# Kernel optimization log

Measured on AMD Instinct MI355X. Metric: run time of the kernel, lower is better.

## Reference

```python
import jax, jax.numpy as jnp
import numpy as np


def setup_inputs() -> dict:
    key = jax.random.key(0)
    k1, k2, k3, k4 = jax.random.split(key, 4)
    S, B = 64000, 64
    audio = jax.random.normal(k1, (S, B), dtype=jnp.float32)
    g = jax.random.uniform(k2, (S, B, 1), dtype=jnp.float32)
    twoR = jax.random.uniform(k3, (S, B, 1), dtype=jnp.float32)
    mix = jax.random.uniform(k4, (S, B, 3), dtype=jnp.float32)
    return {"audio": audio, "g": g, "twoR": twoR, "mix": mix}


def reference(audio, g, twoR, mix):
    # audio: [S, B]; g, twoR: [S, B, 1]; mix: [S, B, 3]
    S, B = audio.shape
    T = 1.0 / (1.0 + g * (g + twoR))                      # [S, B, 1]
    ones = jnp.ones_like(g)
    # Time-varying 2x2 transition matrix H[t, b] = T * [[1, -g], [g, 2Rg+1]]
    H = T[..., None] * jnp.concatenate(
        [ones, -g, g, twoR * g + 1.0], axis=-1).reshape(S, B, 2, 2)
    gHB = g * T * jnp.concatenate([ones, g], axis=-1)     # [S, B, 2]
    gHBx = gHB * audio[..., None]                         # [S, B, 2]

    def step(state, inp):
        # state: [B, 2]; Ht: [B, 2, 2]; bt: [B, 2]
        Ht, bt = inp
        Yt = bt + jnp.einsum('bij,bj->bi', Ht, state)
        return 2.0 * Yt - state, Yt

    state0 = jnp.ones((B, 2), dtype=audio.dtype)
    _, Y = jax.lax.scan(step, state0, (H, gHBx))          # Y: [S, B, 2]

    twoR2 = twoR[..., 0]                                  # [S, B]
    y_hps = audio - twoR2 * Y[..., 0] - Y[..., 1]
    y_mixed = (twoR2 * mix[..., 0] * Y[..., 0]
               + mix[..., 1] * Y[..., 1]
               + mix[..., 2] * y_hps)
    return y_mixed.T                                      # [B, S]
```

## Files before the change

### kernel.cpp

```cpp
#include <hip/hip_runtime.h>

#define S_LEN  64000
#define B_N    64
#define MCH    8
#define WPB    8
#define BSTEPS (MCH * WPB)
#define NBLK   (S_LEN / BSTEPS)
#define KPL    4
#define SCAN_T 256

struct Aff { float m00, m01, m10, m11, v0, v1; };

__device__ __forceinline__ Aff aff_id() {
    Aff r; r.m00 = 1.f; r.m01 = 0.f; r.m10 = 0.f; r.m11 = 1.f; r.v0 = 0.f; r.v1 = 0.f;
    return r;
}

__device__ __forceinline__ Aff aff_comp(const Aff& X, const Aff& Y) {
    Aff r;
    r.m00 = fmaf(X.m00, Y.m00, X.m01 * Y.m10);
    r.m01 = fmaf(X.m00, Y.m01, X.m01 * Y.m11);
    r.m10 = fmaf(X.m10, Y.m00, X.m11 * Y.m10);
    r.m11 = fmaf(X.m10, Y.m01, X.m11 * Y.m11);
    r.v0  = fmaf(X.m00, Y.v0, fmaf(X.m01, Y.v1, X.v0));
    r.v1  = fmaf(X.m10, Y.v0, fmaf(X.m11, Y.v1, X.v1));
    return r;
}

__device__ __forceinline__ Aff svf_step(float g, float R, float x) {
    Aff a;
    float T  = 1.0f / fmaf(g, g + R, 1.0f);
    float gT = g * T;
    a.m00 = fmaf(2.0f, T, -1.0f);
    a.m01 = -2.0f * gT;
    a.m10 =  2.0f * gT;
    a.m11 = fmaf(2.0f, fmaf(R, gT, T), -1.0f);
    a.v0  = a.m10 * x;
    a.v1  = g * a.v0;
    return a;
}

__device__ __forceinline__ void aff_store_lds(float* p, const Aff& a) {
    p[0] = a.m00; p[1] = a.m01; p[2] = a.m10; p[3] = a.m11; p[4] = a.v0; p[5] = a.v1;
}
__device__ __forceinline__ Aff aff_load_lds(const float* p) {
    Aff a; a.m00 = p[0]; a.m01 = p[1]; a.m10 = p[2]; a.m11 = p[3]; a.v0 = p[4]; a.v1 = p[5];
    return a;
}
__device__ __forceinline__ void aff_store_g(float2* p, const Aff& a) {
    p[0] = make_float2(a.m00, a.m01);
    p[1] = make_float2(a.m10, a.m11);
    p[2] = make_float2(a.v0,  a.v1);
}
__device__ __forceinline__ Aff aff_load_g(const float2* p) {
    float2 x = p[0], y = p[1], z = p[2];
    Aff a; a.m00 = x.x; a.m01 = x.y; a.m10 = y.x; a.m11 = y.y; a.v0 = z.x; a.v1 = z.y;
    return a;
}

__global__ __launch_bounds__(512) void k_macro(
    const float* __restrict__ audio, const float* __restrict__ g,
    const float* __restrict__ twoR, float2* __restrict__ wsMac)
{
    __shared__ float affs[WPB * B_N * 7];
    const int b   = threadIdx.x & 63;
    const int w   = threadIdx.x >> 6;
    const int blk = blockIdx.x;
    const int base = (blk * BSTEPS + w * MCH) * B_N + b;

    Aff acc = aff_id();
#pragma unroll
    for (int i = 0; i < MCH; ++i) {
        const int idx = base + i * B_N;
        acc = aff_comp(svf_step(g[idx], twoR[idx], audio[idx]), acc);
    }
    aff_store_lds(&affs[(w * B_N + b) * 7], acc);
    __syncthreads();

    if (w == 0) {
        Aff M = acc;
#pragma unroll
        for (int j = 1; j < WPB; ++j) {
            Aff A = aff_load_lds(&affs[(j * B_N + b) * 7]);
            M = aff_comp(A, M);
        }
        aff_store_g(&wsMac[(blk * B_N + b) * 3], M);
    }
}

__global__ __launch_bounds__(SCAN_T) void k_scan(
    const float2* __restrict__ wsMac, float2* __restrict__ sIn)
{
    const int b    = blockIdx.x;
    const int t    = threadIdx.x;
    const int lane = t & 63;
    const int wave = t >> 6;

    Aff cM[KPL];
#pragma unroll
    for (int k = 0; k < KPL; ++k) {
        const int p = t * KPL + k;
        cM[k] = (p < NBLK) ? aff_load_g(&wsMac[(p * B_N + b) * 3]) : aff_id();
    }

    Aff acc = aff_id();
#pragma unroll
    for (int k = 0; k < KPL; ++k) acc = aff_comp(cM[k], acc);

#pragma unroll
    for (int d = 1; d < 64; d <<= 1) {
        Aff o;
        o.m00 = __shfl_up(acc.m00, (unsigned)d, 64);
        o.m01 = __shfl_up(acc.m01, (unsigned)d, 64);
        o.m10 = __shfl_up(acc.m10, (unsigned)d, 64);
        o.m11 = __shfl_up(acc.m11, (unsigned)d, 64);
        o.v0  = __shfl_up(acc.v0,  (unsigned)d, 64);
        o.v1  = __shfl_up(acc.v1,  (unsigned)d, 64);
        if (lane >= d) acc = aff_comp(acc, o);
    }

    __shared__ Aff wt[SCAN_T / 64];
    if (lane == 63) wt[wave] = acc;
    __syncthreads();

    Aff E;
    E.m00 = __shfl_up(acc.m00, 1u, 64);
    E.m01 = __shfl_up(acc.m01, 1u, 64);
    E.m10 = __shfl_up(acc.m10, 1u, 64);
    E.m11 = __shfl_up(acc.m11, 1u, 64);
    E.v0  = __shfl_up(acc.v0,  1u, 64);
    E.v1  = __shfl_up(acc.v1,  1u, 64);
    if (lane == 0) E = aff_id();

    Aff P = aff_id();
    for (int j = 0; j < wave; ++j) P = aff_comp(wt[j], P);
    E = aff_comp(E, P);

    float s0 = E.m00 + E.m01 + E.v0;
    float s1 = E.m10 + E.m11 + E.v1;

#pragma unroll
    for (int k = 0; k < KPL; ++k) {
        const int p = t * KPL + k;
        if (p < NBLK) {
            sIn[p * B_N + b] = make_float2(s0, s1);
            float n0 = fmaf(cM[k].m00, s0, fmaf(cM[k].m01, s1, cM[k].v0));
            float n1 = fmaf(cM[k].m10, s0, fmaf(cM[k].m11, s1, cM[k].v1));
            s0 = n0; s1 = n1;
        }
    }
}

__global__ __launch_bounds__(512) void k_replay(
    const float* __restrict__ audio, const float* __restrict__ g,
    const float* __restrict__ twoR, const float* __restrict__ mix,
    const float2* __restrict__ sIn, float* __restrict__ out)
{
    __shared__ float lds[BSTEPS * 65];
    const int b   = threadIdx.x & 63;
    const int w   = threadIdx.x >> 6;
    const int blk = blockIdx.x;
    const int base = (blk * BSTEPS + w * MCH) * B_N + b;

    float gv[MCH], Rv[MCH], xv[MCH], m0v[MCH], m1v[MCH], m2v[MCH];
#pragma unroll
    for (int i = 0; i < MCH; ++i) {
        const int idx = base + i * B_N;
        gv[i] = g[idx]; Rv[i] = twoR[idx]; xv[i] = audio[idx];
        m0v[i] = mix[idx * 3]; m1v[i] = mix[idx * 3 + 1]; m2v[i] = mix[idx * 3 + 2];
    }

    Aff acc = aff_id();
#pragma unroll
    for (int i = 0; i < MCH; ++i)
        acc = aff_comp(svf_step(gv[i], Rv[i], xv[i]), acc);
    aff_store_lds(&lds[(w * B_N + b) * 7], acc);
    __syncthreads();

    float2 sm = sIn[blk * B_N + b];
    Aff P = aff_id();
    for (int j = 0; j < w; ++j) {
        Aff A = aff_load_lds(&lds[(j * B_N + b) * 7]);
        P = aff_comp(A, P);
    }
    float s0 = fmaf(P.m00, sm.x, fmaf(P.m01, sm.y, P.v0));
    float s1 = fmaf(P.m10, sm.x, fmaf(P.m11, sm.y, P.v1));
    __syncthreads();

#pragma unroll
    for (int i = 0; i < MCH; ++i) {
        float gg = gv[i], R = Rv[i], x = xv[i];
        float T  = 1.0f / fmaf(gg, gg + R, 1.0f);
        float gT = gg * T;
        float b0 = gT * x;
        float b1 = gg * b0;
        float Y0 = fmaf(T, s0, fmaf(-gT, s1, b0));
        float Y1 = fmaf(gT, s0, fmaf(fmaf(R, gT, T), s1, b1));
        s0 = fmaf(2.0f, Y0, -s0);
        s1 = fmaf(2.0f, Y1, -s1);

        float yh = x - fmaf(R, Y0, Y1);
        float y  = fmaf(R * m0v[i], Y0, fmaf(m1v[i], Y1, m2v[i] * yh));

        lds[(w * MCH + i) * 65 + b] = y;
    }
    __syncthreads();

    const int col = threadIdx.x & 63;
    const int r0  = threadIdx.x >> 6;
    const int colbase = blk * BSTEPS;
#pragma unroll
    for (int r = r0; r < B_N; r += WPB) {
        out[r * S_LEN + colbase + col] = lds[col * 65 + r];
    }
}

extern "C" void kernel_launch(void* const* d_in, const int* in_sizes, int n_in,
                              void* d_out, int out_size, void* d_ws, size_t ws_size,
                              hipStream_t stream)
{
    const float* audio = (const float*)d_in[0];
    const float* g     = (const float*)d_in[1];
    const float* twoR  = (const float*)d_in[2];
    const float* mix   = (const float*)d_in[3];
    float* out = (float*)d_out;

    float2* wsMac = (float2*)d_ws;
    float2* sIn   = wsMac + NBLK * B_N * 3;

    k_macro <<<dim3(NBLK), dim3(512), 0, stream>>>(audio, g, twoR, wsMac);
    k_scan  <<<dim3(B_N), dim3(SCAN_T), 0, stream>>>(wsMac, sIn);
    k_replay<<<dim3(NBLK), dim3(512), 0, stream>>>(audio, g, twoR, mix, sIn, out);
}
```

Measured before the change: 37.73 us.

## Fuse macro, scan and replay passes into one cooperative kernel with grid syncs

```diff
diff --git a/kernel.cpp b/kernel.cpp
--- a/kernel.cpp
+++ b/kernel.cpp
@@ -1,13 +1,15 @@
 #include <hip/hip_runtime.h>
+#include <hip/hip_cooperative_groups.h>
+
+namespace cg = cooperative_groups;
 
 #define S_LEN  64000
 #define B_N    64
-#define MCH    8
-#define WPB    8
-#define BSTEPS (MCH * WPB)
+#define TPB    1024
+#define WPB    16
+#define MCH    16
+#define BSTEPS (WPB * MCH)
 #define NBLK   (S_LEN / BSTEPS)
-#define KPL    4
-#define SCAN_T 256
 
 struct Aff { float m00, m01, m10, m11, v0, v1; };
 
@@ -58,160 +60,126 @@
     return a;
 }
 
-__global__ __launch_bounds__(512) void k_macro(
+__global__ __launch_bounds__(TPB) void k_fused(
     const float* __restrict__ audio, const float* __restrict__ g,
-    const float* __restrict__ twoR, float2* __restrict__ wsMac)
+    const float* __restrict__ twoR, const float* __restrict__ mix,
+    float2* __restrict__ wsMac, float2* __restrict__ sEntry,
+    float* __restrict__ out)
 {
     __shared__ float affs[WPB * B_N * 7];
+    __shared__ float tile[128 * 65];
+    __shared__ Aff wt[4];
+
     const int b   = threadIdx.x & 63;
     const int w   = threadIdx.x >> 6;
     const int blk = blockIdx.x;
     const int base = (blk * BSTEPS + w * MCH) * B_N + b;
 
-    Aff acc = aff_id();
-#pragma unroll
-    for (int i = 0; i < MCH; ++i) {
-        const int idx = base + i * B_N;
-        acc = aff_comp(svf_step(g[idx], twoR[idx], audio[idx]), acc);
-    }
-    aff_store_lds(&affs[(w * B_N + b) * 7], acc);
-    __syncthreads();
-
-    if (w == 0) {
-        Aff M = acc;
-#pragma unroll
-        for (int j = 1; j < WPB; ++j) {
-            Aff A = aff_load_lds(&affs[(j * B_N + b) * 7]);
-            M = aff_comp(A, M);
-        }
-        aff_store_g(&wsMac[(blk * B_N + b) * 3], M);
-    }
-}
-
-__global__ __launch_bounds__(SCAN_T) void k_scan(
-    const float2* __restrict__ wsMac, float2* __restrict__ sIn)
-{
-    const int b    = blockIdx.x;
-    const int t    = threadIdx.x;
-    const int lane = t & 63;
-    const int wave = t >> 6;
-
-    Aff cM[KPL];
-#pragma unroll
-    for (int k = 0; k < KPL; ++k) {
-        const int p = t * KPL + k;
-        cM[k] = (p < NBLK) ? aff_load_g(&wsMac[(p * B_N + b) * 3]) : aff_id();
-    }
-
-    Aff acc = aff_id();
-#pragma unroll
-    for (int k = 0; k < KPL; ++k) acc = aff_comp(cM[k], acc);
-
-#pragma unroll
-    for (int d = 1; d < 64; d <<= 1) {
-        Aff o;
-        o.m00 = __shfl_up(acc.m00, (unsigned)d, 64);
-        o.m01 = __shfl_up(acc.m01, (unsigned)d, 64);
-        o.m10 = __shfl_up(acc.m10, (unsigned)d, 64);
-        o.m11 = __shfl_up(acc.m11, (unsigned)d, 64);
-        o.v0  = __shfl_up(acc.v0,  (unsigned)d, 64);
-        o.v1  = __shfl_up(acc.v1,  (unsigned)d, 64);
-        if (lane >= d) acc = aff_comp(acc, o);
-    }
-
-    __shared__ Aff wt[SCAN_T / 64];
-    if (lane == 63) wt[wave] = acc;
-    __syncthreads();
-
-    Aff E;
-    E.m00 = __shfl_up(acc.m00, 1u, 64);
-    E.m01 = __shfl_up(acc.m01, 1u, 64);
-    E.m10 = __shfl_up(acc.m10, 1u, 64);
-    E.m11 = __shfl_up(acc.m11, 1u, 64);
-    E.v0  = __shfl_up(acc.v0,  1u, 64);
-    E.v1  = __shfl_up(acc.v1,  1u, 64);
-    if (lane == 0) E = aff_id();
-
-    Aff P = aff_id();
-    for (int j = 0; j < wave; ++j) P = aff_comp(wt[j], P);
-    E = aff_comp(E, P);
-
-    float s0 = E.m00 + E.m01 + E.v0;
-    float s1 = E.m10 + E.m11 + E.v1;
-
-#pragma unroll
-    for (int k = 0; k < KPL; ++k) {
-        const int p = t * KPL + k;
-        if (p < NBLK) {
-            sIn[p * B_N + b] = make_float2(s0, s1);
-            float n0 = fmaf(cM[k].m00, s0, fmaf(cM[k].m01, s1, cM[k].v0));
-            float n1 = fmaf(cM[k].m10, s0, fmaf(cM[k].m11, s1, cM[k].v1));
-            s0 = n0; s1 = n1;
-        }
-    }
-}
-
-__global__ __launch_bounds__(512) void k_replay(
-    const float* __restrict__ audio, const float* __restrict__ g,
-    const float* __restrict__ twoR, const float* __restrict__ mix,
-    const float2* __restrict__ sIn, float* __restrict__ out)
-{
-    __shared__ float lds[BSTEPS * 65];
-    const int b   = threadIdx.x & 63;
-    const int w   = threadIdx.x >> 6;
-    const int blk = blockIdx.x;
-    const int base = (blk * BSTEPS + w * MCH) * B_N + b;
-
-    float gv[MCH], Rv[MCH], xv[MCH], m0v[MCH], m1v[MCH], m2v[MCH];
+    float gv[MCH], Rv[MCH], xv[MCH];
 #pragma unroll
     for (int i = 0; i < MCH; ++i) {
         const int idx = base + i * B_N;
         gv[i] = g[idx]; Rv[i] = twoR[idx]; xv[i] = audio[idx];
-        m0v[i] = mix[idx * 3]; m1v[i] = mix[idx * 3 + 1]; m2v[i] = mix[idx * 3 + 2];
-    }
-
-    Aff acc = aff_id();
-#pragma unroll
-    for (int i = 0; i < MCH; ++i)
-        acc = aff_comp(svf_step(gv[i], Rv[i], xv[i]), acc);
-    aff_store_lds(&lds[(w * B_N + b) * 7], acc);
+    }
+
+    Aff lo = aff_id(), hi = aff_id();
+#pragma unroll
+    for (int i = 0; i < MCH / 2; ++i) {
+        lo = aff_comp(svf_step(gv[i],           Rv[i],           xv[i]),           lo);
+        hi = aff_comp(svf_step(gv[i + MCH / 2], Rv[i + MCH / 2], xv[i + MCH / 2]), hi);
+    }
+    Aff micro = aff_comp(hi, lo);
+    aff_store_lds(&affs[(w * B_N + b) * 7], micro);
     __syncthreads();
 
-    float2 sm = sIn[blk * B_N + b];
+    if (w == 0) {
+        Aff M = micro;
+#pragma unroll
+        for (int j = 1; j < WPB; ++j)
+            M = aff_comp(aff_load_lds(&affs[(j * B_N + b) * 7]), M);
+        aff_store_g(&wsMac[(blk * B_N + b) * 3], M);
+    }
+
+    cg::grid_group grid = cg::this_grid();
+    grid.sync();
+
+    {
+        const bool act = (blk < B_N) && (threadIdx.x < 256);
+        const int t = threadIdx.x, lane = t & 63, wv = t >> 6;
+        Aff acc = aff_id();
+        if (act) {
+            if (t < NBLK) acc = aff_load_g(&wsMac[(t * B_N + blk) * 3]);
+#pragma unroll
+            for (int d = 1; d < 64; d <<= 1) {
+                Aff o;
+                o.m00 = __shfl_up(acc.m00, (unsigned)d, 64);
+                o.m01 = __shfl_up(acc.m01, (unsigned)d, 64);
+                o.m10 = __shfl_up(acc.m10, (unsigned)d, 64);
+                o.m11 = __shfl_up(acc.m11, (unsigned)d, 64);
+                o.v0  = __shfl_up(acc.v0,  (unsigned)d, 64);
+                o.v1  = __shfl_up(acc.v1,  (unsigned)d, 64);
+                if (lane >= d) acc = aff_comp(acc, o);
+            }
+            if (lane == 63) wt[wv] = acc;
+        }
+        __syncthreads();
+        if (act) {
+            Aff E;
+            E.m00 = __shfl_up(acc.m00, 1u, 64);
+            E.m01 = __shfl_up(acc.m01, 1u, 64);
+            E.m10 = __shfl_up(acc.m10, 1u, 64);
+            E.m11 = __shfl_up(acc.m11, 1u, 64);
+            E.v0  = __shfl_up(acc.v0,  1u, 64);
+            E.v1  = __shfl_up(acc.v1,  1u, 64);
+            if (lane == 0) E = aff_id();
+            Aff P = aff_id();
+            for (int j = 0; j < wv; ++j) P = aff_comp(wt[j], P);
+            E = aff_comp(E, P);
+            if (t < NBLK) {
+                float e0 = E.m00 + E.m01 + E.v0;
+                float e1 = E.m10 + E.m11 + E.v1;
+                sEntry[t * B_N + blk] = make_float2(e0, e1);
+            }
+        }
+    }
+    grid.sync();
+
+    float2 sm = sEntry[blk * B_N + b];
     Aff P = aff_id();
-    for (int j = 0; j < w; ++j) {
-        Aff A = aff_load_lds(&lds[(j * B_N + b) * 7]);
-        P = aff_comp(A, P);
-    }
+    for (int j = 0; j < w; ++j)
+        P = aff_comp(aff_load_lds(&affs[(j * B_N + b) * 7]), P);
     float s0 = fmaf(P.m00, sm.x, fmaf(P.m01, sm.y, P.v0));
     float s1 = fmaf(P.m10, sm.x, fmaf(P.m11, sm.y, P.v1));
-    __syncthreads();
-
-#pragma unroll
-    for (int i = 0; i < MCH; ++i) {
-        float gg = gv[i], R = Rv[i], x = xv[i];
-        float T  = 1.0f / fmaf(gg, gg + R, 1.0f);
-        float gT = gg * T;
-        float b0 = gT * x;
-        float b1 = gg * b0;
-        float Y0 = fmaf(T, s0, fmaf(-gT, s1, b0));
-        float Y1 = fmaf(gT, s0, fmaf(fmaf(R, gT, T), s1, b1));
-        s0 = fmaf(2.0f, Y0, -s0);
-        s1 = fmaf(2.0f, Y1, -s1);
-
-        float yh = x - fmaf(R, Y0, Y1);
-        float y  = fmaf(R * m0v[i], Y0, fmaf(m1v[i], Y1, m2v[i] * yh));
-
-        lds[(w * MCH + i) * 65 + b] = y;
-    }
-    __syncthreads();
-
-    const int col = threadIdx.x & 63;
-    const int r0  = threadIdx.x >> 6;
-    const int colbase = blk * BSTEPS;
-#pragma unroll
-    for (int r = r0; r < B_N; r += WPB) {
-        out[r * S_LEN + colbase + col] = lds[col * 65 + r];
+
+    for (int round = 0; round < 2; ++round) {
+        if ((w >> 3) == round) {
+            const int wl = w & 7;
+#pragma unroll
+            for (int i = 0; i < MCH; ++i) {
+                const int idx = base + i * B_N;
+                float m0 = mix[idx * 3], m1 = mix[idx * 3 + 1], m2 = mix[idx * 3 + 2];
+                float gg = gv[i], R = Rv[i], x = xv[i];
+                float T  = 1.0f / fmaf(gg, gg + R, 1.0f);
+                float gT = gg * T;
+                float b0 = gT * x;
+                float b1 = gg * b0;
+                float Y0 = fmaf(T, s0, fmaf(-gT, s1, b0));
+                float Y1 = fmaf(gT, s0, fmaf(fmaf(R, gT, T), s1, b1));
+                s0 = fmaf(2.0f, Y0, -s0);
+                s1 = fmaf(2.0f, Y1, -s1);
+                float yh = x - fmaf(R, Y0, Y1);
+                float y  = fmaf(R * m0, Y0, fmaf(m1, Y1, m2 * yh));
+                tile[(wl * MCH + i) * 65 + b] = y;
+            }
+        }
+        __syncthreads();
+        const int col = threadIdx.x & 127;
+        const int r0  = threadIdx.x >> 7;
+        const int colbase = blk * BSTEPS + round * 128;
+#pragma unroll
+        for (int r = r0; r < B_N; r += 8)
+            out[r * S_LEN + colbase + col] = tile[col * 65 + r];
+        if (round == 0) __syncthreads();
     }
 }
 
@@ -225,10 +193,11 @@
     const float* mix   = (const float*)d_in[3];
     float* out = (float*)d_out;
 
-    float2* wsMac = (float2*)d_ws;
-    float2* sIn   = wsMac + NBLK * B_N * 3;
-
-    k_macro <<<dim3(NBLK), dim3(512), 0, stream>>>(audio, g, twoR, wsMac);
-    k_scan  <<<dim3(B_N), dim3(SCAN_T), 0, stream>>>(wsMac, sIn);
-    k_replay<<<dim3(NBLK), dim3(512), 0, stream>>>(audio, g, twoR, mix, sIn, out);
-}
+    float2* wsMac  = (float2*)d_ws;
+    float2* sEntry = wsMac + NBLK * B_N * 3;
+
+    void* args[] = { (void*)&audio, (void*)&g, (void*)&twoR, (void*)&mix,
+                     (void*)&wsMac, (void*)&sEntry, (void*)&out };
+    hipLaunchCooperativeKernel((void*)k_fused, dim3(NBLK), dim3(TPB),
+                               args, 0, stream);
+}
```

Measured after the change: 132.9 us. 252% more time.
